# Optimization experiments

Measured on AMD Instinct MI355X. Metric: run time of the kernel, lower is better.

The kernel has to match this reference:

```python
import jax, jax.numpy as jnp
import numpy as np

EMBED_DIM = 384


def setup_inputs() -> dict:
    key = jax.random.key(0)
    k1, k2, k3 = jax.random.split(key, 3)
    B, P, N, C = 32, 4, 1024, EMBED_DIM
    x = jax.random.normal(k1, (B, P, N, C), dtype=jnp.float32)
    # 1x1 Conv2D on channel-last == linear on last dim; kernel [Cin, Cout]
    w_qkv = jax.random.normal(k2, (C, 1 + 2 * C), dtype=jnp.float32) * (1.0 / np.sqrt(C))
    b_qkv = jnp.zeros((1 + 2 * C,), dtype=jnp.float32)
    w_proj = jax.random.normal(k3, (C, C), dtype=jnp.float32) * (1.0 / np.sqrt(C))
    b_proj = jnp.zeros((C,), dtype=jnp.float32)
    return {"x": x, "w_qkv": w_qkv, "b_qkv": b_qkv, "w_proj": w_proj, "b_proj": b_proj}


def reference(x, w_qkv, b_qkv, w_proj, b_proj):
    C = EMBED_DIM
    # qkv pointwise conv: [B,P,N,C] @ [C, 1+2C]
    qkv = jnp.einsum('bpnc,cd->bpnd', x, w_qkv) + b_qkv
    query = qkv[..., :1]                 # [B,P,N,1]
    key_t = qkv[..., 1:1 + C]            # [B,P,N,C]
    value = qkv[..., 1 + C:]             # [B,P,N,C]
    # NOTE: softmax over the trailing axis of size 1 (faithful to source) -> all ones
    context_scores = jax.nn.softmax(query, axis=-1)
    # key * scores, reduce-sum over patch-index axis (axis=2), keepdims
    context_vector = jnp.sum(key_t * context_scores, axis=2, keepdims=True)  # [B,P,1,C]
    gated = jax.nn.relu(value) * context_vector                              # [B,P,N,C]
    out = jnp.einsum('bpnc,cd->bpnd', gated, w_proj) + b_proj
    return out
```

## Files before the change

### kernel.cpp

```cpp
#include <hip/hip_runtime.h>
#include <hip/hip_bf16.h>
#include <type_traits>
#include <utility>

#define C_    384
#define N_    1024
#define G_    128
#define QKVD  769
#define SPLIT 16

typedef float  f32x4 __attribute__((ext_vector_type(4)));
typedef short  s16x8 __attribute__((ext_vector_type(8)));
typedef __bf16 b16x8 __attribute__((ext_vector_type(8)));

template <typename V, typename = void>
struct mfma_takes : std::false_type {};
template <typename V>
struct mfma_takes<V, std::void_t<decltype(__builtin_amdgcn_mfma_f32_16x16x32_bf16(
    std::declval<V>(), std::declval<V>(), std::declval<f32x4>(), 0, 0, 0))>>
    : std::true_type {};

using frag_t = std::conditional_t<mfma_takes<s16x8>::value, s16x8, b16x8>;

template <typename V>
__device__ __forceinline__ f32x4 mfma_bf16(V a, V b, f32x4 c) {
  return __builtin_amdgcn_mfma_f32_16x16x32_bf16(a, b, c, 0, 0, 0);
}

__device__ __forceinline__ unsigned short f2bf(float f) {
  union { float f; unsigned u; } v; v.f = f;
  unsigned r = v.u + 0x7fffu + ((v.u >> 16) & 1u);
  return (unsigned short)(r >> 16);
}

__global__ void k_xsum(const float* __restrict__ x, float* __restrict__ xsum) {
  int g = blockIdx.x >> 4;
  int s = blockIdx.x & (SPLIT - 1);
  int c = threadIdx.x;
  const float* p = x + ((size_t)g * N_ + (size_t)s * (N_ / SPLIT)) * C_ + c;
  float acc = 0.f;
#pragma unroll 8
  for (int r = 0; r < N_ / SPLIT; ++r) acc += p[(size_t)r * C_];
  atomicAdd(&xsum[g * C_ + c], acc);
}

__global__ void k_cv(const float* __restrict__ xsum, const float* __restrict__ w_qkv,
                     const float* __restrict__ b_qkv, float* __restrict__ cv) {
  __shared__ float xs[C_];
  int g = blockIdx.x, c = threadIdx.x;
  xs[c] = xsum[g * C_ + c];
  __syncthreads();
  float acc = 0.f;
#pragma unroll 4
  for (int k = 0; k < C_; ++k) acc += xs[k] * w_qkv[k * QKVD + 1 + c];
  cv[g * C_ + c] = acc + (float)N_ * b_qkv[1 + c];
}

__global__ void k_pack(const float* __restrict__ w_qkv, const float* __restrict__ w_proj,
                       unsigned short* __restrict__ pWv, unsigned short* __restrict__ pWp) {
  int bid = blockIdx.x;
  int mat = bid / 288;
  int r   = bid % 288;
  int kk = r / 24, nf = r % 24;
  int lane = threadIdx.x;
  int kbase = kk * 32 + (lane >> 4) * 8;
  int n = nf * 16 + (lane & 15);
  unsigned v[4];
#pragma unroll
  for (int jj = 0; jj < 4; ++jj) {
    int k0 = kbase + jj * 2;
    float f0 = mat ? w_proj[(size_t)k0 * C_ + n]       : w_qkv[(size_t)k0 * QKVD + 385 + n];
    float f1 = mat ? w_proj[(size_t)(k0 + 1) * C_ + n] : w_qkv[(size_t)(k0 + 1) * QKVD + 385 + n];
    v[jj] = (unsigned)f2bf(f0) | ((unsigned)f2bf(f1) << 16);
  }
  unsigned short* dst = (mat ? pWp : pWv) + ((size_t)r * 64 + lane) * 8;
  uint4 w; w.x = v[0]; w.y = v[1]; w.z = v[2]; w.w = v[3];
  *(uint4*)dst = w;
}

__global__ __launch_bounds__(256) void k_fused(
    const float* __restrict__ x, const unsigned short* __restrict__ pWv,
    const unsigned short* __restrict__ pWp, const float* __restrict__ cv,
    const float* __restrict__ b_qkv, const float* __restrict__ b_proj,
    float* __restrict__ out) {
  __shared__ __align__(16) char tile[64 * 768];
  __shared__ float cv_l[C_], bv_l[C_], bp_l[C_];

  const int tid  = threadIdx.x;
  const int lane = tid & 63;
  const int wv   = tid >> 6;
  const int R0   = blockIdx.x * 64;
  const int g    = R0 >> 10;

  for (int c = tid; c < C_; c += 256) {
    cv_l[c] = cv[g * C_ + c];
    bv_l[c] = b_qkv[1 + C_ + c];
    bp_l[c] = b_proj[c];
  }

  {
    const float* xg = x + (size_t)R0 * C_;
#pragma unroll
    for (int i = 0; i < 12; ++i) {
      int ch  = i * 256 + tid;
      int row = ch / 48;
      int col = (ch % 48) * 8;
      const float4* s0 = (const float4*)(xg + (size_t)row * C_ + col);
      float4 a = s0[0], b = s0[1];
      uint4 w;
      w.x = (unsigned)f2bf(a.x) | ((unsigned)f2bf(a.y) << 16);
      w.y = (unsigned)f2bf(a.z) | ((unsigned)f2bf(a.w) << 16);
      w.z = (unsigned)f2bf(b.x) | ((unsigned)f2bf(b.y) << 16);
      w.w = (unsigned)f2bf(b.z) | ((unsigned)f2bf(b.w) << 16);
      int byte = row * 768 + col * 2;
      byte ^= (row & 7) << 4;
      *(uint4*)(tile + byte) = w;
    }
  }
  __syncthreads();

  const int wcol = wv * 96;
  const f32x4 zero = {0.f, 0.f, 0.f, 0.f};
  f32x4 acc[4][6];
#pragma unroll
  for (int m = 0; m < 4; ++m)
#pragma unroll
    for (int n = 0; n < 6; ++n) acc[m][n] = zero;

  for (int kk = 0; kk < 12; ++kk) {
    frag_t A[4], Bv[6];
    int kb2 = (kk * 32 + (lane >> 4) * 8) * 2;
#pragma unroll
    for (int m = 0; m < 4; ++m) {
      int row = m * 16 + (lane & 15);
      int byte = row * 768 + kb2;
      byte ^= (row & 7) << 4;
      A[m] = *(const frag_t*)(tile + byte);
    }
    const unsigned short* bp_ = pWv + ((size_t)(kk * 24 + wv * 6) * 64 + lane) * 8;
#pragma unroll
    for (int n = 0; n < 6; ++n) Bv[n] = *(const frag_t*)(bp_ + (size_t)n * 64 * 8);
#pragma unroll
    for (int m = 0; m < 4; ++m)
#pragma unroll
      for (int n = 0; n < 6; ++n) acc[m][n] = mfma_bf16(A[m], Bv[n], acc[m][n]);
  }

  __syncthreads();

#pragma unroll
  for (int m = 0; m < 4; ++m) {
#pragma unroll
    for (int n = 0; n < 6; ++n) {
      int col = wcol + n * 16 + (lane & 15);
      float cvv = cv_l[col], bvv = bv_l[col];
#pragma unroll
      for (int r = 0; r < 4; ++r) {
        int row = m * 16 + (lane >> 4) * 4 + r;
        float val = acc[m][n][r] + bvv;
        val = fmaxf(val, 0.f) * cvv;
        int byte = row * 768 + col * 2;
        byte ^= (row & 7) << 4;
        *(unsigned short*)(tile + byte) = f2bf(val);
      }
    }
  }
  __syncthreads();

  f32x4 acc2[4][6];
#pragma unroll
  for (int m = 0; m < 4; ++m)
#pragma unroll
    for (int n = 0; n < 6; ++n) acc2[m][n] = zero;

  for (int kk = 0; kk < 12; ++kk) {
    frag_t A[4], Bv[6];
    int kb2 = (kk * 32 + (lane >> 4) * 8) * 2;
#pragma unroll
    for (int m = 0; m < 4; ++m) {
      int row = m * 16 + (lane & 15);
      int byte = row * 768 + kb2;
      byte ^= (row & 7) << 4;
      A[m] = *(const frag_t*)(tile + byte);
    }
    const unsigned short* bp_ = pWp + ((size_t)(kk * 24 + wv * 6) * 64 + lane) * 8;
#pragma unroll
    for (int n = 0; n < 6; ++n) Bv[n] = *(const frag_t*)(bp_ + (size_t)n * 64 * 8);
#pragma unroll
    for (int m = 0; m < 4; ++m)
#pragma unroll
      for (int n = 0; n < 6; ++n) acc2[m][n] = mfma_bf16(A[m], Bv[n], acc2[m][n]);
  }

#pragma unroll
  for (int m = 0; m < 4; ++m) {
#pragma unroll
    for (int n = 0; n < 6; ++n) {
      int col = wcol + n * 16 + (lane & 15);
      float bpv = bp_l[col];
#pragma unroll
      for (int r = 0; r < 4; ++r) {
        int row = m * 16 + (lane >> 4) * 4 + r;
        out[(size_t)(R0 + row) * C_ + col] = acc2[m][n][r] + bpv;
      }
    }
  }
}

extern "C" void kernel_launch(void* const* d_in, const int* in_sizes, int n_in,
                              void* d_out, int out_size, void* d_ws, size_t ws_size,
                              hipStream_t stream) {
  const float* x      = (const float*)d_in[0];
  const float* w_qkv  = (const float*)d_in[1];
  const float* b_qkv  = (const float*)d_in[2];
  const float* w_proj = (const float*)d_in[3];
  const float* b_proj = (const float*)d_in[4];
  float* out = (float*)d_out;

  float* xsum = (float*)d_ws;
  float* cvp  = xsum + G_ * C_;
  unsigned short* pWv = (unsigned short*)(cvp + G_ * C_);
  unsigned short* pWp = pWv + C_ * C_;

  hipMemsetAsync(xsum, 0, G_ * C_ * sizeof(float), stream);
  k_pack<<<576, 64, 0, stream>>>(w_qkv, w_proj, pWv, pWp);
  k_xsum<<<G_ * SPLIT, C_, 0, stream>>>(x, xsum);
  k_cv<<<G_, C_, 0, stream>>>(xsum, w_qkv, b_qkv, cvp);
  k_fused<<<2048, 256, 0, stream>>>(x, pWv, pWp, cvp, b_qkv, b_proj, out);
}
```

Baseline: 268.0 us.

## Precompute bf16 copy of x during column-sum pass and DMA it into LDS

A new prep kernel reads x once, writes a bf16 copy to workspace and computes the per-group column sums through shared-memory atomics, replacing the separate xsum pass. When the workspace is large enough, the fused kernel then stages the bf16 tile straight into LDS with global_load_lds, applying the swizzle on the source address, and skips the in-kernel conversion. This trades an extra bf16 write plus read (half of x's size) against halving the fused kernel's input traffic and removing conversion work. It also adds launch_bounds occupancy hints and reuses one accumulator array. Whether this path runs depends on ws_size.

```diff
diff --git a/kernel.cpp b/kernel.cpp
--- a/kernel.cpp
+++ b/kernel.cpp
@@ -7,7 +7,6 @@
 #define N_    1024
 #define G_    128
 #define QKVD  769
-#define SPLIT 16
 
 typedef float  f32x4 __attribute__((ext_vector_type(4)));
 typedef short  s16x8 __attribute__((ext_vector_type(8)));
@@ -32,15 +31,62 @@
   unsigned r = v.u + 0x7fffu + ((v.u >> 16) & 1u);
   return (unsigned short)(r >> 16);
 }
+__device__ __forceinline__ unsigned pack2(float lo, float hi) {
+  return (unsigned)f2bf(lo) | ((unsigned)f2bf(hi) << 16);
+}
+
+__device__ __forceinline__ void stage16(const char* g, char* lbase, int lane) {
+#if __has_builtin(__builtin_amdgcn_global_load_lds)
+  __builtin_amdgcn_global_load_lds(
+      (const __attribute__((address_space(1))) void*)g,
+      (__attribute__((address_space(3))) void*)lbase, 16, 0, 0);
+#else
+  *(uint4*)(lbase + lane * 16) = *(const uint4*)g;
+#endif
+}
+
+__global__ __launch_bounds__(192) void k_prep(const float* __restrict__ x,
+                                              unsigned short* __restrict__ xb,
+                                              float* __restrict__ xsum) {
+  __shared__ float csum[C_];
+  const int b = blockIdx.x;
+  const int g = b >> 4;
+  const int tid = threadIdx.x;
+  const int col8 = (tid % 48) * 8;
+  const int rgrp = tid / 48;
+  for (int c = tid; c < C_; c += 192) csum[c] = 0.f;
+  __syncthreads();
+  const size_t base = (size_t)b * 64 + (size_t)rgrp * 16;
+  const float* xp = x + base * C_ + col8;
+  unsigned short* xbp = xb + base * C_ + col8;
+  float s[8];
+#pragma unroll
+  for (int j = 0; j < 8; ++j) s[j] = 0.f;
+#pragma unroll 4
+  for (int r = 0; r < 16; ++r) {
+    float4 a = *(const float4*)(xp + (size_t)r * C_);
+    float4 c = *(const float4*)(xp + (size_t)r * C_ + 4);
+    uint4 w;
+    w.x = pack2(a.x, a.y); w.y = pack2(a.z, a.w);
+    w.z = pack2(c.x, c.y); w.w = pack2(c.z, c.w);
+    *(uint4*)(xbp + (size_t)r * C_) = w;
+    s[0] += a.x; s[1] += a.y; s[2] += a.z; s[3] += a.w;
+    s[4] += c.x; s[5] += c.y; s[6] += c.z; s[7] += c.w;
+  }
+#pragma unroll
+  for (int j = 0; j < 8; ++j) atomicAdd(&csum[col8 + j], s[j]);
+  __syncthreads();
+  for (int c = tid; c < C_; c += 192) atomicAdd(&xsum[g * C_ + c], csum[c]);
+}
 
 __global__ void k_xsum(const float* __restrict__ x, float* __restrict__ xsum) {
   int g = blockIdx.x >> 4;
-  int s = blockIdx.x & (SPLIT - 1);
+  int s = blockIdx.x & 15;
   int c = threadIdx.x;
-  const float* p = x + ((size_t)g * N_ + (size_t)s * (N_ / SPLIT)) * C_ + c;
+  const float* p = x + ((size_t)g * N_ + (size_t)s * 64) * C_ + c;
   float acc = 0.f;
 #pragma unroll 8
-  for (int r = 0; r < N_ / SPLIT; ++r) acc += p[(size_t)r * C_];
+  for (int r = 0; r < 64; ++r) acc += p[(size_t)r * C_];
   atomicAdd(&xsum[g * C_ + c], acc);
 }
 
@@ -78,11 +124,12 @@
   *(uint4*)dst = w;
 }
 
-__global__ __launch_bounds__(256) void k_fused(
-    const float* __restrict__ x, const unsigned short* __restrict__ pWv,
-    const unsigned short* __restrict__ pWp, const float* __restrict__ cv,
-    const float* __restrict__ b_qkv, const float* __restrict__ b_proj,
-    float* __restrict__ out) {
+template <bool PRE>
+__global__ __launch_bounds__(256, 4) void k_fused(
+    const float* __restrict__ x, const unsigned short* __restrict__ xb,
+    const unsigned short* __restrict__ pWv, const unsigned short* __restrict__ pWp,
+    const float* __restrict__ cv, const float* __restrict__ b_qkv,
+    const float* __restrict__ b_proj, float* __restrict__ out) {
   __shared__ __align__(16) char tile[64 * 768];
   __shared__ float cv_l[C_], bv_l[C_], bp_l[C_];
 
@@ -98,7 +145,18 @@
     bp_l[c] = b_proj[c];
   }
 
-  {
+  if constexpr (PRE) {
+    const char* xg = (const char*)(xb + (size_t)R0 * C_);
+#pragma unroll
+    for (int i = 0; i < 12; ++i) {
+      int idx = wv * 12 + i;
+      int L   = idx * 1024 + lane * 16;
+      int row = L / 768;
+      int cbs = L - row * 768;
+      int src = row * 768 + (cbs ^ ((row & 7) << 4));
+      stage16(xg + src, tile + idx * 1024, lane);
+    }
+  } else {
     const float* xg = x + (size_t)R0 * C_;
 #pragma unroll
     for (int i = 0; i < 12; ++i) {
@@ -108,10 +166,8 @@
       const float4* s0 = (const float4*)(xg + (size_t)row * C_ + col);
       float4 a = s0[0], b = s0[1];
       uint4 w;
-      w.x = (unsigned)f2bf(a.x) | ((unsigned)f2bf(a.y) << 16);
-      w.y = (unsigned)f2bf(a.z) | ((unsigned)f2bf(a.w) << 16);
-      w.z = (unsigned)f2bf(b.x) | ((unsigned)f2bf(b.y) << 16);
-      w.w = (unsigned)f2bf(b.z) | ((unsigned)f2bf(b.w) << 16);
+      w.x = pack2(a.x, a.y); w.y = pack2(a.z, a.w);
+      w.z = pack2(b.x, b.y); w.w = pack2(b.z, b.w);
       int byte = row * 768 + col * 2;
       byte ^= (row & 7) << 4;
       *(uint4*)(tile + byte) = w;
@@ -133,8 +189,7 @@
 #pragma unroll
     for (int m = 0; m < 4; ++m) {
       int row = m * 16 + (lane & 15);
-      int byte = row * 768 + kb2;
-      byte ^= (row & 7) << 4;
+      int byte = (row * 768 + kb2) ^ ((row & 7) << 4);
       A[m] = *(const frag_t*)(tile + byte);
     }
     const unsigned short* bp_ = pWv + ((size_t)(kk * 24 + wv * 6) * 64 + lane) * 8;
@@ -159,19 +214,17 @@
         int row = m * 16 + (lane >> 4) * 4 + r;
         float val = acc[m][n][r] + bvv;
         val = fmaxf(val, 0.f) * cvv;
-        int byte = row * 768 + col * 2;
-        byte ^= (row & 7) << 4;
+        int byte = (row * 768 + col * 2) ^ ((row & 7) << 4);
         *(unsigned short*)(tile + byte) = f2bf(val);
       }
     }
   }
   __syncthreads();
 
-  f32x4 acc2[4][6];
 #pragma unroll
   for (int m = 0; m < 4; ++m)
 #pragma unroll
-    for (int n = 0; n < 6; ++n) acc2[m][n] = zero;
+    for (int n = 0; n < 6; ++n) acc[m][n] = zero;
 
   for (int kk = 0; kk < 12; ++kk) {
     frag_t A[4], Bv[6];
@@ -179,8 +232,7 @@
 #pragma unroll
     for (int m = 0; m < 4; ++m) {
       int row = m * 16 + (lane & 15);
-      int byte = row * 768 + kb2;
-      byte ^= (row & 7) << 4;
+      int byte = (row * 768 + kb2) ^ ((row & 7) << 4);
       A[m] = *(const frag_t*)(tile + byte);
     }
     const unsigned short* bp_ = pWp + ((size_t)(kk * 24 + wv * 6) * 64 + lane) * 8;
@@ -189,7 +241,7 @@
 #pragma unroll
     for (int m = 0; m < 4; ++m)
 #pragma unroll
-      for (int n = 0; n < 6; ++n) acc2[m][n] = mfma_bf16(A[m], Bv[n], acc2[m][n]);
+      for (int n = 0; n < 6; ++n) acc[m][n] = mfma_bf16(A[m], Bv[n], acc[m][n]);
   }
 
 #pragma unroll
@@ -201,7 +253,7 @@
 #pragma unroll
       for (int r = 0; r < 4; ++r) {
         int row = m * 16 + (lane >> 4) * 4 + r;
-        out[(size_t)(R0 + row) * C_ + col] = acc2[m][n][r] + bpv;
+        out[(size_t)(R0 + row) * C_ + col] = acc[m][n][r] + bpv;
       }
     }
   }
@@ -221,10 +273,21 @@
   float* cvp  = xsum + G_ * C_;
   unsigned short* pWv = (unsigned short*)(cvp + G_ * C_);
   unsigned short* pWp = pWv + C_ * C_;
+  unsigned short* xb  = pWp + C_ * C_;
+
+  const size_t small_bytes = (size_t)G_ * C_ * 4 * 2 + (size_t)C_ * C_ * 2 * 2;
+  const size_t need = small_bytes + (size_t)G_ * N_ * C_ * 2;
 
   hipMemsetAsync(xsum, 0, G_ * C_ * sizeof(float), stream);
   k_pack<<<576, 64, 0, stream>>>(w_qkv, w_proj, pWv, pWp);
-  k_xsum<<<G_ * SPLIT, C_, 0, stream>>>(x, xsum);
-  k_cv<<<G_, C_, 0, stream>>>(xsum, w_qkv, b_qkv, cvp);
-  k_fused<<<2048, 256, 0, stream>>>(x, pWv, pWp, cvp, b_qkv, b_proj, out);
-}
+
+  if (ws_size >= need) {
+    k_prep<<<2048, 192, 0, stream>>>(x, xb, xsum);
+    k_cv<<<G_, C_, 0, stream>>>(xsum, w_qkv, b_qkv, cvp);
+    k_fused<true><<<2048, 256, 0, stream>>>(x, xb, pWv, pWp, cvp, b_qkv, b_proj, out);
+  } else {
+    k_xsum<<<G_ * 16, C_, 0, stream>>>(x, xsum);
+    k_cv<<<G_, C_, 0, stream>>>(xsum, w_qkv, b_qkv, cvp);
+    k_fused<false><<<2048, 256, 0, stream>>>(x, xb, pWv, pWp, cvp, b_qkv, b_proj, out);
+  }
+}
```

After: 285.3 us. 1.06x slower.

## Make fused kernel persistent over row tiles with double-buffered register prefetch

Applied to the files above, without the earlier changes.

The fused GEMM kernel now launches 512 blocks of 512 threads. Each block loops over eight 32-row tiles and prefetches the next x tile into registers while it computes on the current one, staging it into a second LDS buffer. The xsum reduction is changed to vectorized float4 loads with an in-block shared-memory reduction, which cuts the number of atomics. The smaller per-wave tiles (2x3 MFMA fragments) lower reuse of B fragments per load, and the prefetch registers add register pressure.

```diff
diff --git a/kernel.cpp b/kernel.cpp
--- a/kernel.cpp
+++ b/kernel.cpp
@@ -7,7 +7,6 @@
 #define N_    1024
 #define G_    128
 #define QKVD  769
-#define SPLIT 16
 
 typedef float  f32x4 __attribute__((ext_vector_type(4)));
 typedef short  s16x8 __attribute__((ext_vector_type(8)));
@@ -32,16 +31,34 @@
   unsigned r = v.u + 0x7fffu + ((v.u >> 16) & 1u);
   return (unsigned short)(r >> 16);
 }
-
-__global__ void k_xsum(const float* __restrict__ x, float* __restrict__ xsum) {
-  int g = blockIdx.x >> 4;
-  int s = blockIdx.x & (SPLIT - 1);
-  int c = threadIdx.x;
-  const float* p = x + ((size_t)g * N_ + (size_t)s * (N_ / SPLIT)) * C_ + c;
-  float acc = 0.f;
+__device__ __forceinline__ unsigned pack2(float lo, float hi) {
+  return (unsigned)f2bf(lo) | ((unsigned)f2bf(hi) << 16);
+}
+
+__global__ __launch_bounds__(384) void k_xsum(const float* __restrict__ x,
+                                              float* __restrict__ xsum) {
+  __shared__ float sh[4][C_];
+  const int tid = threadIdx.x;
+  const int c4  = (tid % 96) * 4;
+  const int rg  = tid / 96;
+  const int b   = blockIdx.x;
+  const int g   = b >> 3;
+  const float* p = x + ((size_t)b * 128 + (size_t)rg * 32) * C_ + c4;
+  f32x4 s = {0.f, 0.f, 0.f, 0.f};
 #pragma unroll 8
-  for (int r = 0; r < N_ / SPLIT; ++r) acc += p[(size_t)r * C_];
-  atomicAdd(&xsum[g * C_ + c], acc);
+  for (int r = 0; r < 32; ++r) {
+    float4 v = *(const float4*)(p + (size_t)r * C_);
+    s.x += v.x; s.y += v.y; s.z += v.z; s.w += v.w;
+  }
+  *(f32x4*)&sh[rg][c4] = s;
+  __syncthreads();
+  if (rg == 0) {
+#pragma unroll
+    for (int j = 0; j < 4; ++j) {
+      float v = sh[0][c4 + j] + sh[1][c4 + j] + sh[2][c4 + j] + sh[3][c4 + j];
+      atomicAdd(&xsum[g * C_ + c4 + j], v);
+    }
+  }
 }
 
 __global__ void k_cv(const float* __restrict__ xsum, const float* __restrict__ w_qkv,
@@ -78,133 +95,139 @@
   *(uint4*)dst = w;
 }
 
-__global__ __launch_bounds__(256) void k_fused(
+__global__ __launch_bounds__(512, 4) void k_fused(
     const float* __restrict__ x, const unsigned short* __restrict__ pWv,
     const unsigned short* __restrict__ pWp, const float* __restrict__ cv,
     const float* __restrict__ b_qkv, const float* __restrict__ b_proj,
     float* __restrict__ out) {
-  __shared__ __align__(16) char tile[64 * 768];
+  __shared__ __align__(16) char tile[2][32 * 768];
   __shared__ float cv_l[C_], bv_l[C_], bp_l[C_];
 
   const int tid  = threadIdx.x;
   const int lane = tid & 63;
   const int wv   = tid >> 6;
-  const int R0   = blockIdx.x * 64;
-  const int g    = R0 >> 10;
-
-  for (int c = tid; c < C_; c += 256) {
+  const int g    = blockIdx.x >> 2;
+  const size_t blockRow0 = (size_t)blockIdx.x * 256;
+  const float* xblk = x + blockRow0 * C_;
+
+  for (int c = tid; c < C_; c += 512) {
     cv_l[c] = cv[g * C_ + c];
     bv_l[c] = b_qkv[1 + C_ + c];
     bp_l[c] = b_proj[c];
   }
 
-  {
-    const float* xg = x + (size_t)R0 * C_;
-#pragma unroll
-    for (int i = 0; i < 12; ++i) {
-      int ch  = i * 256 + tid;
-      int row = ch / 48;
-      int col = (ch % 48) * 8;
-      const float4* s0 = (const float4*)(xg + (size_t)row * C_ + col);
-      float4 a = s0[0], b = s0[1];
-      uint4 w;
-      w.x = (unsigned)f2bf(a.x) | ((unsigned)f2bf(a.y) << 16);
-      w.y = (unsigned)f2bf(a.z) | ((unsigned)f2bf(a.w) << 16);
-      w.z = (unsigned)f2bf(b.x) | ((unsigned)f2bf(b.y) << 16);
-      w.w = (unsigned)f2bf(b.z) | ((unsigned)f2bf(b.w) << 16);
-      int byte = row * 768 + col * 2;
-      byte ^= (row & 7) << 4;
-      *(uint4*)(tile + byte) = w;
-    }
-  }
+  float4 pf[6];
+#define LOADT(xt)                                                         \
+  _Pragma("unroll") for (int j = 0; j < 3; ++j) {                         \
+    pf[2 * j]     = *(const float4*)((xt) + ((size_t)tid + j * 512) * 8); \
+    pf[2 * j + 1] = *(const float4*)((xt) + ((size_t)tid + j * 512) * 8 + 4); \
+  }
+#define STAGET(buf)                                                       \
+  _Pragma("unroll") for (int j = 0; j < 3; ++j) {                         \
+    int ch  = tid + j * 512;                                              \
+    int row = ch / 48;                                                    \
+    int off = (ch % 48) * 16;                                             \
+    uint4 w;                                                              \
+    w.x = pack2(pf[2 * j].x, pf[2 * j].y);                                \
+    w.y = pack2(pf[2 * j].z, pf[2 * j].w);                                \
+    w.z = pack2(pf[2 * j + 1].x, pf[2 * j + 1].y);                        \
+    w.w = pack2(pf[2 * j + 1].z, pf[2 * j + 1].w);                        \
+    *(uint4*)(tile[buf] + row * 768 + (off ^ ((row & 7) << 4))) = w;      \
+  }
+
+  LOADT(xblk);
+  STAGET(0);
   __syncthreads();
 
-  const int wcol = wv * 96;
   const f32x4 zero = {0.f, 0.f, 0.f, 0.f};
-  f32x4 acc[4][6];
-#pragma unroll
-  for (int m = 0; m < 4; ++m)
-#pragma unroll
-    for (int n = 0; n < 6; ++n) acc[m][n] = zero;
-
-  for (int kk = 0; kk < 12; ++kk) {
-    frag_t A[4], Bv[6];
-    int kb2 = (kk * 32 + (lane >> 4) * 8) * 2;
-#pragma unroll
-    for (int m = 0; m < 4; ++m) {
-      int row = m * 16 + (lane & 15);
-      int byte = row * 768 + kb2;
-      byte ^= (row & 7) << 4;
-      A[m] = *(const frag_t*)(tile + byte);
-    }
-    const unsigned short* bp_ = pWv + ((size_t)(kk * 24 + wv * 6) * 64 + lane) * 8;
-#pragma unroll
-    for (int n = 0; n < 6; ++n) Bv[n] = *(const frag_t*)(bp_ + (size_t)n * 64 * 8);
-#pragma unroll
-    for (int m = 0; m < 4; ++m)
-#pragma unroll
-      for (int n = 0; n < 6; ++n) acc[m][n] = mfma_bf16(A[m], Bv[n], acc[m][n]);
-  }
-
-  __syncthreads();
-
-#pragma unroll
-  for (int m = 0; m < 4; ++m) {
-#pragma unroll
-    for (int n = 0; n < 6; ++n) {
-      int col = wcol + n * 16 + (lane & 15);
-      float cvv = cv_l[col], bvv = bv_l[col];
-#pragma unroll
-      for (int r = 0; r < 4; ++r) {
-        int row = m * 16 + (lane >> 4) * 4 + r;
-        float val = acc[m][n][r] + bvv;
-        val = fmaxf(val, 0.f) * cvv;
-        int byte = row * 768 + col * 2;
-        byte ^= (row & 7) << 4;
-        *(unsigned short*)(tile + byte) = f2bf(val);
-      }
-    }
-  }
-  __syncthreads();
-
-  f32x4 acc2[4][6];
-#pragma unroll
-  for (int m = 0; m < 4; ++m)
-#pragma unroll
-    for (int n = 0; n < 6; ++n) acc2[m][n] = zero;
-
-  for (int kk = 0; kk < 12; ++kk) {
-    frag_t A[4], Bv[6];
-    int kb2 = (kk * 32 + (lane >> 4) * 8) * 2;
-#pragma unroll
-    for (int m = 0; m < 4; ++m) {
-      int row = m * 16 + (lane & 15);
-      int byte = row * 768 + kb2;
-      byte ^= (row & 7) << 4;
-      A[m] = *(const frag_t*)(tile + byte);
-    }
-    const unsigned short* bp_ = pWp + ((size_t)(kk * 24 + wv * 6) * 64 + lane) * 8;
-#pragma unroll
-    for (int n = 0; n < 6; ++n) Bv[n] = *(const frag_t*)(bp_ + (size_t)n * 64 * 8);
-#pragma unroll
-    for (int m = 0; m < 4; ++m)
-#pragma unroll
-      for (int n = 0; n < 6; ++n) acc2[m][n] = mfma_bf16(A[m], Bv[n], acc2[m][n]);
-  }
-
-#pragma unroll
-  for (int m = 0; m < 4; ++m) {
-#pragma unroll
-    for (int n = 0; n < 6; ++n) {
-      int col = wcol + n * 16 + (lane & 15);
-      float bpv = bp_l[col];
-#pragma unroll
-      for (int r = 0; r < 4; ++r) {
-        int row = m * 16 + (lane >> 4) * 4 + r;
-        out[(size_t)(R0 + row) * C_ + col] = acc2[m][n][r] + bpv;
-      }
-    }
-  }
+
+#pragma unroll 1
+  for (int t = 0; t < 8; ++t) {
+    const int cur = t & 1;
+
+    if (t < 7) { LOADT(xblk + (size_t)(t + 1) * 32 * C_); }
+
+    f32x4 acc[2][3];
+#pragma unroll
+    for (int m = 0; m < 2; ++m)
+#pragma unroll
+      for (int n = 0; n < 3; ++n) acc[m][n] = zero;
+
+    for (int kk = 0; kk < 12; ++kk) {
+      frag_t A[2], Bv[3];
+      int kb2 = (kk * 32 + (lane >> 4) * 8) * 2;
+#pragma unroll
+      for (int m = 0; m < 2; ++m) {
+        int row = m * 16 + (lane & 15);
+        A[m] = *(const frag_t*)(tile[cur] + ((row * 768 + kb2) ^ ((row & 7) << 4)));
+      }
+      const unsigned short* bp_ = pWv + ((size_t)(kk * 24 + wv * 3) * 64 + lane) * 8;
+#pragma unroll
+      for (int n = 0; n < 3; ++n) Bv[n] = *(const frag_t*)(bp_ + (size_t)n * 64 * 8);
+#pragma unroll
+      for (int m = 0; m < 2; ++m)
+#pragma unroll
+        for (int n = 0; n < 3; ++n) acc[m][n] = mfma_bf16(A[m], Bv[n], acc[m][n]);
+    }
+    __syncthreads();
+
+#pragma unroll
+    for (int m = 0; m < 2; ++m) {
+#pragma unroll
+      for (int n = 0; n < 3; ++n) {
+        int col = wv * 48 + n * 16 + (lane & 15);
+        float cvv = cv_l[col], bvv = bv_l[col];
+#pragma unroll
+        for (int r = 0; r < 4; ++r) {
+          int row = m * 16 + (lane >> 4) * 4 + r;
+          float val = fmaxf(acc[m][n][r] + bvv, 0.f) * cvv;
+          *(unsigned short*)(tile[cur] + ((row * 768 + col * 2) ^ ((row & 7) << 4))) = f2bf(val);
+        }
+      }
+    }
+    __syncthreads();
+
+#pragma unroll
+    for (int m = 0; m < 2; ++m)
+#pragma unroll
+      for (int n = 0; n < 3; ++n) acc[m][n] = zero;
+
+    for (int kk = 0; kk < 12; ++kk) {
+      frag_t A[2], Bv[3];
+      int kb2 = (kk * 32 + (lane >> 4) * 8) * 2;
+#pragma unroll
+      for (int m = 0; m < 2; ++m) {
+        int row = m * 16 + (lane & 15);
+        A[m] = *(const frag_t*)(tile[cur] + ((row * 768 + kb2) ^ ((row & 7) << 4)));
+      }
+      const unsigned short* bp_ = pWp + ((size_t)(kk * 24 + wv * 3) * 64 + lane) * 8;
+#pragma unroll
+      for (int n = 0; n < 3; ++n) Bv[n] = *(const frag_t*)(bp_ + (size_t)n * 64 * 8);
+#pragma unroll
+      for (int m = 0; m < 2; ++m)
+#pragma unroll
+        for (int n = 0; n < 3; ++n) acc[m][n] = mfma_bf16(A[m], Bv[n], acc[m][n]);
+    }
+
+#pragma unroll
+    for (int m = 0; m < 2; ++m) {
+#pragma unroll
+      for (int n = 0; n < 3; ++n) {
+        int col = wv * 48 + n * 16 + (lane & 15);
+        float bpv = bp_l[col];
+#pragma unroll
+        for (int r = 0; r < 4; ++r) {
+          int row = m * 16 + (lane >> 4) * 4 + r;
+          out[(blockRow0 + (size_t)t * 32 + row) * C_ + col] = acc[m][n][r] + bpv;
+        }
+      }
+    }
+
+    if (t < 7) { STAGET(cur ^ 1); }
+    __syncthreads();
+  }
+#undef LOADT
+#undef STAGET
 }
 
 extern "C" void kernel_launch(void* const* d_in, const int* in_sizes, int n_in,
@@ -223,8 +246,8 @@
   unsigned short* pWp = pWv + C_ * C_;
 
   hipMemsetAsync(xsum, 0, G_ * C_ * sizeof(float), stream);
+  k_xsum<<<1024, 384, 0, stream>>>(x, xsum);
   k_pack<<<576, 64, 0, stream>>>(w_qkv, w_proj, pWv, pWp);
-  k_xsum<<<G_ * SPLIT, C_, 0, stream>>>(x, xsum);
   k_cv<<<G_, C_, 0, stream>>>(xsum, w_qkv, b_qkv, cvp);
-  k_fused<<<2048, 256, 0, stream>>>(x, pWv, pWp, cvp, b_qkv, b_proj, out);
-}
+  k_fused<<<512, 512, 0, stream>>>(x, pWv, pWp, cvp, b_qkv, b_proj, out);
+}
```

Result: slower. 923.0 us (+244.4%).
